# Kernel optimization log

Hardware: AMD Instinct MI355X
Metric: run time of the kernel (lower is better)

The kernel has to match this reference:

```python
import jax, jax.numpy as jnp
import numpy as np

# --- dims / constants ---
T, N, SD, TD, A, H = 64, 512, 64, 64, 32, 2048
REPEAT = 2
IN_DIM = SD + TD
DT, TAU_MEM, TAU_SYN = 1e-3, 5e-3, 2e-3
DCY_M = float(np.exp(-DT / TAU_MEM))   # membrane decay exp(-dt/tau_mem)
DCY_S = float(np.exp(-DT / TAU_SYN))   # synaptic decay exp(-dt/tau_syn)
SCL_M = 1.0 - DCY_M
BETA = 100.0  # SigmoidSpike surrogate steepness

@jax.custom_vjp
def spike(x):
    # forward: hard threshold (binary spike)
    return (x > 0).astype(x.dtype)

def _spike_fwd(x):
    return spike(x), x

def _spike_bwd(x, g):
    s = jax.nn.sigmoid(BETA * x)
    return (g * BETA * s * (1.0 - s),)

spike.defvjp(_spike_fwd, _spike_bwd)

def setup_inputs() -> dict:
    key = jax.random.key(0)
    ks = jax.random.split(key, 8)
    f32 = jnp.float32
    state = jax.random.normal(ks[0], (T, N, SD), dtype=f32)
    target = jax.random.normal(ks[1], (T, N, TD), dtype=f32)
    # fluctuation-driven centered-normal init ~ N(0, 1/fan_in)
    Wi = jax.random.normal(ks[2], (IN_DIM, H), dtype=f32) / np.sqrt(IN_DIM)
    bi = jnp.zeros((H,), dtype=f32)
    Vr = jax.random.normal(ks[3], (H, H), dtype=f32) / np.sqrt(H)
    Wf = jax.random.normal(ks[4], (H, H), dtype=f32) / np.sqrt(H)
    bf = jnp.zeros((H,), dtype=f32)
    Wo = jax.random.normal(ks[5], (H, 2 * A), dtype=f32) / np.sqrt(H)
    bo = jnp.zeros((2 * A,), dtype=f32)
    return {"state": state, "target": target, "Wi": Wi, "bi": bi,
            "Vr": Vr, "Wf": Wf, "bf": bf, "Wo": Wo, "bo": bo}

def _run(state, target, Wi, bi, Vr, Wf, bf, Wo, bo):
    x_seq = jnp.concatenate([state, target], axis=-1)        # (T, N, IN_DIM)
    x_seq = jnp.repeat(x_seq, REPEAT, axis=0)                 # (T*REPEAT, N, IN_DIM)

    def step(carry, xt):
        syn1, mem1, s1, syn2, mem2, s2, synr, memr = carry
        # recurrent LIF layer: feedforward + recurrent input
        I1 = xt @ Wi + bi + s1 @ Vr
        nmem1 = (DCY_M * mem1 + SCL_M * syn1) * (1.0 - s1)    # reset by last spikes
        nsyn1 = DCY_S * syn1 + I1
        ns1 = spike(nmem1 - 1.0)                              # threshold = 1
        # feedforward LIF layer
        I2 = ns1 @ Wf + bf
        nmem2 = (DCY_M * mem2 + SCL_M * syn2) * (1.0 - s2)
        nsyn2 = DCY_S * syn2 + I2
        ns2 = spike(nmem2 - 1.0)
        # non-spiking readout pool (leaky integrator)
        Ir = ns2 @ Wo + bo
        nmemr = DCY_M * memr + SCL_M * synr
        nsynr = DCY_S * synr + Ir
        new_carry = (nsyn1, nmem1, ns1, nsyn2, nmem2, ns2, nsynr, nmemr)
        return new_carry, nmemr

    z = lambda d: jnp.zeros((N, d), dtype=state.dtype)
    carry0 = (z(H), z(H), z(H), z(H), z(H), z(H), z(2 * A), z(2 * A))
    _, ro = jax.lax.scan(step, carry0, x_seq)                 # (T*REPEAT, N, 2A)
    # TimeAverageReadoutGroup: mean over the repeat_input micro-steps
    ro = ro.reshape(T, REPEAT, N, 2 * A).mean(axis=1)         # (T, N, 2A)
    mu, logvar = jnp.split(ro, 2, axis=-1)
    return mu, logvar

def reference(state, target, Wi, bi, Vr, Wf, bf, Wo, bo):
    return _run(state, target, Wi, bi, Vr, Wf, bf, Wo, bo)
```

## Files before the change

### kernel.cpp

```cpp
#include <hip/hip_runtime.h>
#include <stdint.h>


typedef unsigned long long u64;
typedef unsigned int u32;
typedef float f32x4 __attribute__((ext_vector_type(4)));

#define NB 512
#define HD 2048
#define NSTEPS 128
#define THREADS 512
#define NBLK 256
#define COLS 256
#define SPB 16
#define NWPS 32
#define LSTN 1024

#define DMc 0.8187307530779818f
#define DSc 0.6065306597126334f
#define SMc 0.18126924692201818f

#define OFF_M1W 0
#define SZ_M1W (2 * NB * NWPS * 8)
#define OFF_M2H (OFF_M1W + SZ_M1W)
#define SZ_M2H ((size_t)NSTEPS * NB * NWPS * 8)
#define OFF_FLAG (OFF_M2H + SZ_M2H)
#define SZ_FLAG (32 * 32 * 4)
#define OFF_CNT (OFF_FLAG + SZ_FLAG)
#define OFF_DONE (OFF_CNT + 64)
#define OFF_PK (((size_t)(OFF_DONE + 4) + 4194303) & ~(size_t)4194303)
#define SZ_PK ((size_t)8 * HD * 512 * 4)

#define HWREG_XCC_ID (20 | ((4 - 1) << 11))

__global__ void init_ws(u64* __restrict__ m1W, u32* __restrict__ flags,
                        u32* __restrict__ cnt, u32* __restrict__ done) {
  int i = blockIdx.x * 256 + threadIdx.x;
  if (i < 2 * NB * NWPS) m1W[i] = 0ULL;
  if (i < 32 * 32) flags[i] = 0u;
  if (i < 8) cnt[i] = 0u;
  if (i == 0) *done = 0u;
}

__global__ __launch_bounds__(256) void pack_kernel(
    const float* __restrict__ Vr, const float* __restrict__ Wf,
    float* __restrict__ PK) {
  const int k = blockIdx.x;
  const int tid = threadIdx.x;
  for (int c = tid; c < HD; c += 256) {
    int xcd = c >> 8, cc = c & 255;
    size_t base = ((size_t)xcd * HD + k) * 512;
    __builtin_nontemporal_store(Vr[(size_t)k * HD + c], &PK[base + cc]);
    __builtin_nontemporal_store(Wf[(size_t)k * HD + c], &PK[base + 256 + cc]);
  }
}

__device__ __forceinline__ u64 spread4(u64 x) {
  x &= 0xffffULL;
  x = (x | (x << 24)) & 0x000000FF000000FFULL;
  x = (x | (x << 12)) & 0x000F000F000F000FULL;
  x = (x | (x << 6))  & 0x0303030303030303ULL;
  x = (x | (x << 3))  & 0x1111111111111111ULL;
  return x;
}

__device__ __forceinline__ u64 pack_word(u64 B0, u64 B1, u64 B2, u64 B3, int q) {
  int sh = q * 16;
  return spread4(B0 >> sh) | (spread4(B1 >> sh) << 1) |
         (spread4(B2 >> sh) << 2) | (spread4(B3 >> sh) << 3);
}

template <bool ATOMIC>
__device__ __forceinline__ int build_list(const u64* __restrict__ mwords,
                                          uint16_t* __restrict__ lstw, int lane) {
  u64 w = 0ULL;
  if (lane < NWPS) {
    if (ATOMIC)
      w = __hip_atomic_load((u64*)&mwords[lane], __ATOMIC_RELAXED,
                            __HIP_MEMORY_SCOPE_AGENT);
    else
      w = mwords[lane];
  }
  int pc = __popcll(w);
  int pre = pc;
#pragma unroll
  for (int off = 1; off < 64; off <<= 1) {
    int v = __shfl_up(pre, off);
    if (lane >= off) pre += v;
  }
  int excl = pre - pc;
  int total = __shfl(pre, 63);
  int kb = lane << 6;
  while (w) {
    int b = __builtin_ctzll(w);
    w &= w - 1;
    if (excl < LSTN) lstw[excl] = (uint16_t)(kb + b);
    ++excl;
  }
  asm volatile("s_waitcnt lgkmcnt(0)" ::: "memory");
  return total < LSTN ? total : LSTN;
}

__device__ __forceinline__ void dual_gather_pk(const float* __restrict__ PKb,
                                               const uint16_t* __restrict__ lstw,
                                               int total, float aV[4],
                                               float aW[4]) {
  for (int j0 = 0; j0 < total; j0 += 8) {
    f32x4 va[8], vb[8];
#pragma unroll
    for (int u = 0; u < 8; ++u) {
      int idx = j0 + u;
      if (idx >= total) idx = j0;
      size_t off = ((size_t)lstw[idx]) << 9;
      va[u] = *(const f32x4*)(PKb + off);
      vb[u] = *(const f32x4*)(PKb + off + 256);
    }
#pragma unroll
    for (int u = 0; u < 8; ++u)
      if (j0 + u < total) {
        aV[0] += va[u].x; aV[1] += va[u].y; aV[2] += va[u].z; aV[3] += va[u].w;
        aW[0] += vb[u].x; aW[1] += vb[u].y; aW[2] += vb[u].z; aW[3] += vb[u].w;
      }
  }
}

__device__ __forceinline__ u32 lif_update(const float acc[4], float syn[4],
                                          float mem[4], u32 snib) {
  u32 nib = 0;
#pragma unroll
  for (int j = 0; j < 4; ++j) {
    float so = (float)((snib >> j) & 1u);
    float nmem = (DMc * mem[j] + SMc * syn[j]) * (1.0f - so);
    float nsyn = DSc * syn[j] + acc[j];
    mem[j] = nmem;
    syn[j] = nsyn;
    if ((nmem - 1.0f) > 0.0f) nib |= (1u << j);
  }
  return nib;
}

__global__ __launch_bounds__(THREADS) void rsnn_coop(
    const float* __restrict__ state, const float* __restrict__ target,
    const float* __restrict__ Wi, const float* __restrict__ bi,
    const float* __restrict__ Vr, const float* __restrict__ Wf,
    const float* __restrict__ bf, const float* __restrict__ Wo,
    const float* __restrict__ bo, float* __restrict__ out,
    char* __restrict__ wsb) {
  __shared__ float Wi_s[128 * COLS];
  __shared__ uint16_t lst[8][LSTN];
  __shared__ int sh_xcd, sh_rank;

  u64* m1W = (u64*)(wsb + OFF_M1W);
  u64* m2H = (u64*)(wsb + OFF_M2H);
  u32* flags = (u32*)(wsb + OFF_FLAG);
  u32* cnt = (u32*)(wsb + OFF_CNT);
  u32* done = (u32*)(wsb + OFF_DONE);
  const float* PK = (const float*)(wsb + OFF_PK);

  const int tid = threadIdx.x;
  const int wv = tid >> 6;
  const int lane = tid & 63;

  if (tid == 0) {
    int xcd = __builtin_amdgcn_s_getreg(HWREG_XCC_ID) & 7;
    sh_xcd = xcd;
    sh_rank = atomicAdd(&cnt[xcd], 1u) & 31;
  }
  __syncthreads();
  const int xcd = sh_xcd;
  const int g = sh_rank;
  const int c0 = xcd * COLS;
  const int sA = g * SPB + wv * 2, sB = sA + 1;

  for (int i = tid; i < 128 * COLS; i += THREADS) {
    int k = i >> 8, c = i & 255;
    Wi_s[i] = Wi[(size_t)k * HD + c0 + c];
  }

  float bir[4], bfr[4];
#pragma unroll
  for (int j = 0; j < 4; ++j) {
    bir[j] = bi[c0 + lane * 4 + j];
    bfr[j] = bf[c0 + lane * 4 + j];
  }

  float syn1[2][4], mem1[2][4], syn2[2][4], mem2[2][4];
#pragma unroll
  for (int r = 0; r < 2; ++r)
#pragma unroll
    for (int j = 0; j < 4; ++j) {
      syn1[r][j] = 0.f; mem1[r][j] = 0.f; syn2[r][j] = 0.f; mem2[r][j] = 0.f;
    }
  u32 s1nib[2] = {0u, 0u}, s2nib[2] = {0u, 0u};
  float xwA[4], xwB[4];

  const float* PKb = PK + (size_t)xcd * HD * 512 + lane * 4;
  u32* myflag = &flags[g * 32];

  __syncthreads();

  auto compute_xw = [&](int t2) {
#pragma unroll
    for (int j = 0; j < 4; ++j) { xwA[j] = bir[j]; xwB[j] = bir[j]; }
#pragma unroll
    for (int half = 0; half < 2; ++half) {
      const float* pA = (half ? target : state) + ((size_t)t2 * NB + sA) * 64;
      const float* pB = (half ? target : state) + ((size_t)t2 * NB + sB) * 64;
      for (int q = 0; q < 16; ++q) {
        f32x4 xa = *(const f32x4*)(pA + 4 * q);
        f32x4 xb = *(const f32x4*)(pB + 4 * q);
        float xav[4] = {xa.x, xa.y, xa.z, xa.w};
        float xbv[4] = {xb.x, xb.y, xb.z, xb.w};
#pragma unroll
        for (int kj = 0; kj < 4; ++kj) {
          const f32x4 w4 =
              *(const f32x4*)&Wi_s[(half * 64 + 4 * q + kj) * COLS + lane * 4];
          xwA[0] = fmaf(xav[kj], w4.x, xwA[0]);
          xwA[1] = fmaf(xav[kj], w4.y, xwA[1]);
          xwA[2] = fmaf(xav[kj], w4.z, xwA[2]);
          xwA[3] = fmaf(xav[kj], w4.w, xwA[3]);
          xwB[0] = fmaf(xbv[kj], w4.x, xwB[0]);
          xwB[1] = fmaf(xbv[kj], w4.y, xwB[1]);
          xwB[2] = fmaf(xbv[kj], w4.z, xwB[2]);
          xwB[3] = fmaf(xbv[kj], w4.w, xwB[3]);
        }
      }
    }
  };

  compute_xw(0);
#pragma unroll
  for (int r = 0; r < 2; ++r) {
    const int smp = r ? sB : sA;
    s1nib[r] = lif_update(r ? xwB : xwA, syn1[r], mem1[r], s1nib[r]);
    u64 B0 = __ballot(s1nib[r] & 1u), B1 = __ballot(s1nib[r] & 2u);
    u64 B2 = __ballot(s1nib[r] & 4u), B3 = __ballot(s1nib[r] & 8u);
    if (lane < 4) {
      u64 wd = pack_word(B0, B1, B2, B3, lane);
      __hip_atomic_store(&m1W[(size_t)smp * NWPS + 4 * xcd + lane], wd,
                         __ATOMIC_RELAXED, __HIP_MEMORY_SCOPE_AGENT);
    }
  }
  __syncthreads();
  if (tid == 0) {
    __hip_atomic_fetch_add(myflag, 1u, __ATOMIC_RELAXED, __HIP_MEMORY_SCOPE_AGENT);
    while (__hip_atomic_load(myflag, __ATOMIC_RELAXED,
                             __HIP_MEMORY_SCOPE_AGENT) < 8u)
      __builtin_amdgcn_s_sleep(2);
  }
  __syncthreads();

  for (int s = 0; s < NSTEPS; ++s) {
    if (s + 1 < NSTEPS && ((s + 1) & 1) == 0) compute_xw((s + 1) >> 1);

    const u64* m1cur = m1W + (size_t)(s & 1) * NB * NWPS;
    u64* m1nxt = m1W + (size_t)((s + 1) & 1) * NB * NWPS;
    const bool last = (s == NSTEPS - 1);

#pragma unroll
    for (int r = 0; r < 2; ++r) {
      const int smp = r ? sB : sA;
      int tot = build_list<true>(m1cur + (size_t)smp * NWPS, &lst[wv][0], lane);

      float aV[4], aW[4];
#pragma unroll
      for (int j = 0; j < 4; ++j) {
        aV[j] = r ? xwB[j] : xwA[j];
        aW[j] = bfr[j];
      }
      dual_gather_pk(PKb, &lst[wv][0], tot, aV, aW);

      s2nib[r] = lif_update(aW, syn2[r], mem2[r], s2nib[r]);
      {
        u64 B0 = __ballot(s2nib[r] & 1u), B1 = __ballot(s2nib[r] & 2u);
        u64 B2 = __ballot(s2nib[r] & 4u), B3 = __ballot(s2nib[r] & 8u);
        if (lane < 4) {
          u64 wd = pack_word(B0, B1, B2, B3, lane);
          __hip_atomic_store(
              &m2H[((size_t)s * NB + smp) * NWPS + 4 * xcd + lane], wd,
              __ATOMIC_RELAXED, __HIP_MEMORY_SCOPE_AGENT);
        }
      }
      if (!last) {
        s1nib[r] = lif_update(aV, syn1[r], mem1[r], s1nib[r]);
        u64 B0 = __ballot(s1nib[r] & 1u), B1 = __ballot(s1nib[r] & 2u);
        u64 B2 = __ballot(s1nib[r] & 4u), B3 = __ballot(s1nib[r] & 8u);
        if (lane < 4) {
          u64 wd = pack_word(B0, B1, B2, B3, lane);
          __hip_atomic_store(&m1nxt[(size_t)smp * NWPS + 4 * xcd + lane], wd,
                             __ATOMIC_RELAXED, __HIP_MEMORY_SCOPE_AGENT);
        }
      }
    }

    if (!last) {
      __syncthreads();
      if (tid == 0) {
        __hip_atomic_fetch_add(myflag, 1u, __ATOMIC_RELAXED,
                               __HIP_MEMORY_SCOPE_AGENT);
        u32 tgt = 8u * (u32)(s + 2);
        while (__hip_atomic_load(myflag, __ATOMIC_RELAXED,
                                 __HIP_MEMORY_SCOPE_AGENT) < tgt)
          __builtin_amdgcn_s_sleep(2);
      }
      __syncthreads();
    }
  }

  __syncthreads();
  if (tid == 0) {
    __threadfence();
    __hip_atomic_fetch_add(done, 1u, __ATOMIC_RELEASE, __HIP_MEMORY_SCOPE_AGENT);
    while (__hip_atomic_load(done, __ATOMIC_RELAXED,
                             __HIP_MEMORY_SCOPE_AGENT) < (u32)NBLK)
      __builtin_amdgcn_s_sleep(8);
    __threadfence();
  }
  __syncthreads();

  if (wv < 2) {
    const int rsmp = blockIdx.x * 2 + wv;
    const float bor = bo[lane];
    float synr = 0.f, memr = 0.f, roprev = 0.f;
    for (int s = 0; s < NSTEPS; ++s) {
      int total = build_list<false>(m2H + ((size_t)s * NB + rsmp) * NWPS,
                                    &lst[wv][0], lane);
      float a = bor;
      for (int j0 = 0; j0 < total; j0 += 8) {
        float vv[8];
#pragma unroll
        for (int u = 0; u < 8; ++u) {
          int idx = j0 + u;
          if (idx >= total) idx = j0;
          vv[u] = Wo[(((size_t)lst[wv][idx]) << 6) + lane];
        }
#pragma unroll
        for (int u = 0; u < 8; ++u)
          if (j0 + u < total) a += vv[u];
      }
      float nmemr = DMc * memr + SMc * synr;
      float nsynr = DSc * synr + a;
      memr = nmemr;
      synr = nsynr;
      if (s & 1) {
        float v = 0.5f * (roprev + nmemr);
        size_t base = ((size_t)(s >> 1) * NB + rsmp) * 32;
        if (lane < 32) out[base + lane] = v;
        else out[(size_t)64 * NB * 32 + base + (lane - 32)] = v;
      } else {
        roprev = nmemr;
      }
    }
  }
}

extern "C" void kernel_launch(void* const* d_in, const int* in_sizes, int n_in,
                              void* d_out, int out_size, void* d_ws, size_t ws_size,
                              hipStream_t stream) {
  const float* state  = (const float*)d_in[0];
  const float* target = (const float*)d_in[1];
  const float* Wi     = (const float*)d_in[2];
  const float* bi     = (const float*)d_in[3];
  const float* Vr     = (const float*)d_in[4];
  const float* Wf     = (const float*)d_in[5];
  const float* bf     = (const float*)d_in[6];
  const float* Wo     = (const float*)d_in[7];
  const float* bo     = (const float*)d_in[8];
  float* out = (float*)d_out;
  char* wsb = (char*)d_ws;

  init_ws<<<128, 256, 0, stream>>>((u64*)(wsb + OFF_M1W), (u32*)(wsb + OFF_FLAG),
                                   (u32*)(wsb + OFF_CNT), (u32*)(wsb + OFF_DONE));
  pack_kernel<<<HD, 256, 0, stream>>>(Vr, Wf, (float*)(wsb + OFF_PK));

  void* args[] = {(void*)&state, (void*)&target, (void*)&Wi, (void*)&bi,
                  (void*)&Vr, (void*)&Wf, (void*)&bf, (void*)&Wo, (void*)&bo,
                  (void*)&out, (void*)&wsb};
  (void)hipLaunchCooperativeKernel(rsnn_coop, dim3(NBLK), dim3(THREADS), args, 0,
                                   stream);
}
```

Before: 3.688 ms.

## Replace block barriers with per-sample sequence flags and software-pipeline the gather

Drops the per-step block-wide syncthreads plus counter-flag barrier. Each wave now writes its spike words followed by a per-(sample, XCD) sequence-number flag, and waits only on the eight flags for its own samples. It also builds both samples' spike lists in one pass, double-buffers the gathered PK loads, moves the input projection after the step, and shrinks the list size to fit two list buffers. The aim is to remove block-level serialization and expose memory parallelism. The cost is more polling traffic, reliance on relaxed ordering with vmcnt waits for correctness, and higher register pressure.

```diff
diff --git a/kernel.cpp b/kernel.cpp
--- a/kernel.cpp
+++ b/kernel.cpp
@@ -14,30 +14,27 @@
 #define COLS 256
 #define SPB 16
 #define NWPS 32
-#define LSTN 1024
+#define LSTN 832
 
 #define DMc 0.8187307530779818f
 #define DSc 0.6065306597126334f
 #define SMc 0.18126924692201818f
 
 #define OFF_M1W 0
-#define SZ_M1W (2 * NB * NWPS * 8)
+#define SZ_M1W ((size_t)2 * NB * 8 * 8 * 8)
 #define OFF_M2H (OFF_M1W + SZ_M1W)
 #define SZ_M2H ((size_t)NSTEPS * NB * NWPS * 8)
-#define OFF_FLAG (OFF_M2H + SZ_M2H)
-#define SZ_FLAG (32 * 32 * 4)
-#define OFF_CNT (OFF_FLAG + SZ_FLAG)
+#define OFF_CNT (OFF_M2H + SZ_M2H)
 #define OFF_DONE (OFF_CNT + 64)
 #define OFF_PK (((size_t)(OFF_DONE + 4) + 4194303) & ~(size_t)4194303)
 #define SZ_PK ((size_t)8 * HD * 512 * 4)
 
 #define HWREG_XCC_ID (20 | ((4 - 1) << 11))
 
-__global__ void init_ws(u64* __restrict__ m1W, u32* __restrict__ flags,
-                        u32* __restrict__ cnt, u32* __restrict__ done) {
+__global__ void init_ws(u64* __restrict__ m1W, u32* __restrict__ cnt,
+                        u32* __restrict__ done) {
   int i = blockIdx.x * 256 + threadIdx.x;
-  if (i < 2 * NB * NWPS) m1W[i] = 0ULL;
-  if (i < 32 * 32) flags[i] = 0u;
+  if (i < 2 * NB * 64) m1W[i] = 0ULL;
   if (i < 8) cnt[i] = 0u;
   if (i == 0) *done = 0u;
 }
@@ -70,17 +67,10 @@
          (spread4(B2 >> sh) << 2) | (spread4(B3 >> sh) << 3);
 }
 
-template <bool ATOMIC>
-__device__ __forceinline__ int build_list(const u64* __restrict__ mwords,
-                                          uint16_t* __restrict__ lstw, int lane) {
-  u64 w = 0ULL;
-  if (lane < NWPS) {
-    if (ATOMIC)
-      w = __hip_atomic_load((u64*)&mwords[lane], __ATOMIC_RELAXED,
-                            __HIP_MEMORY_SCOPE_AGENT);
-    else
-      w = mwords[lane];
-  }
+__device__ __forceinline__ int build_list_ro(const u64* __restrict__ mwords,
+                                             uint16_t* __restrict__ lstw,
+                                             int lane) {
+  u64 w = (lane < NWPS) ? mwords[lane] : 0ULL;
   int pc = __popcll(w);
   int pre = pc;
 #pragma unroll
@@ -101,29 +91,6 @@
   return total < LSTN ? total : LSTN;
 }
 
-__device__ __forceinline__ void dual_gather_pk(const float* __restrict__ PKb,
-                                               const uint16_t* __restrict__ lstw,
-                                               int total, float aV[4],
-                                               float aW[4]) {
-  for (int j0 = 0; j0 < total; j0 += 8) {
-    f32x4 va[8], vb[8];
-#pragma unroll
-    for (int u = 0; u < 8; ++u) {
-      int idx = j0 + u;
-      if (idx >= total) idx = j0;
-      size_t off = ((size_t)lstw[idx]) << 9;
-      va[u] = *(const f32x4*)(PKb + off);
-      vb[u] = *(const f32x4*)(PKb + off + 256);
-    }
-#pragma unroll
-    for (int u = 0; u < 8; ++u)
-      if (j0 + u < total) {
-        aV[0] += va[u].x; aV[1] += va[u].y; aV[2] += va[u].z; aV[3] += va[u].w;
-        aW[0] += vb[u].x; aW[1] += vb[u].y; aW[2] += vb[u].z; aW[3] += vb[u].w;
-      }
-  }
-}
-
 __device__ __forceinline__ u32 lif_update(const float acc[4], float syn[4],
                                           float mem[4], u32 snib) {
   u32 nib = 0;
@@ -139,7 +106,57 @@
   return nib;
 }
 
-__global__ __launch_bounds__(THREADS) void rsnn_coop(
+__device__ __forceinline__ void dual_gather_pipe(const float* __restrict__ PKb,
+                                                 const uint16_t* __restrict__ lstw,
+                                                 int tot, float aV[4],
+                                                 float aW[4]) {
+  if (tot <= 0) return;
+  f32x4 vaX[8], vbX[8], vaY[8], vbY[8];
+#define LOADG(VA, VB, J)                                      \
+  {                                                           \
+    _Pragma("unroll") for (int u = 0; u < 8; ++u) {           \
+      int idx = (J) + u;                                      \
+      if (idx >= tot) idx = 0;                                \
+      size_t off = ((size_t)lstw[idx]) << 9;                  \
+      VA[u] = *(const f32x4*)(PKb + off);                     \
+      VB[u] = *(const f32x4*)(PKb + off + 256);               \
+    }                                                         \
+  }
+#define ACCG(VA, VB, J)                                       \
+  {                                                           \
+    _Pragma("unroll") for (int u = 0; u < 8; ++u)             \
+      if ((J) + u < tot) {                                    \
+        aV[0] += VA[u].x; aV[1] += VA[u].y;                   \
+        aV[2] += VA[u].z; aV[3] += VA[u].w;                   \
+        aW[0] += VB[u].x; aW[1] += VB[u].y;                   \
+        aW[2] += VB[u].z; aW[3] += VB[u].w;                   \
+      }                                                       \
+  }
+  int j = 0;
+  LOADG(vaX, vbX, 0);
+  while (true) {
+    if (j + 8 < tot) {
+      LOADG(vaY, vbY, j + 8);
+      ACCG(vaX, vbX, j);
+      j += 8;
+    } else {
+      ACCG(vaX, vbX, j);
+      break;
+    }
+    if (j + 8 < tot) {
+      LOADG(vaX, vbX, j + 8);
+      ACCG(vaY, vbY, j);
+      j += 8;
+    } else {
+      ACCG(vaY, vbY, j);
+      break;
+    }
+  }
+#undef LOADG
+#undef ACCG
+}
+
+__global__ __launch_bounds__(THREADS, 2) void rsnn_coop(
     const float* __restrict__ state, const float* __restrict__ target,
     const float* __restrict__ Wi, const float* __restrict__ bi,
     const float* __restrict__ Vr, const float* __restrict__ Wf,
@@ -147,12 +164,12 @@
     const float* __restrict__ bo, float* __restrict__ out,
     char* __restrict__ wsb) {
   __shared__ float Wi_s[128 * COLS];
-  __shared__ uint16_t lst[8][LSTN];
+  __shared__ uint16_t lstA_s[8][LSTN];
+  __shared__ uint16_t lstB_s[8][LSTN];
   __shared__ int sh_xcd, sh_rank;
 
   u64* m1W = (u64*)(wsb + OFF_M1W);
   u64* m2H = (u64*)(wsb + OFF_M2H);
-  u32* flags = (u32*)(wsb + OFF_FLAG);
   u32* cnt = (u32*)(wsb + OFF_CNT);
   u32* done = (u32*)(wsb + OFF_DONE);
   const float* PK = (const float*)(wsb + OFF_PK);
@@ -162,9 +179,9 @@
   const int lane = tid & 63;
 
   if (tid == 0) {
-    int xcd = __builtin_amdgcn_s_getreg(HWREG_XCC_ID) & 7;
-    sh_xcd = xcd;
-    sh_rank = atomicAdd(&cnt[xcd], 1u) & 31;
+    int x = __builtin_amdgcn_s_getreg(HWREG_XCC_ID) & 7;
+    sh_xcd = x;
+    sh_rank = atomicAdd(&cnt[x], 1u) & 31;
   }
   __syncthreads();
   const int xcd = sh_xcd;
@@ -184,18 +201,19 @@
     bfr[j] = bf[c0 + lane * 4 + j];
   }
 
-  float syn1[2][4], mem1[2][4], syn2[2][4], mem2[2][4];
-#pragma unroll
-  for (int r = 0; r < 2; ++r)
-#pragma unroll
-    for (int j = 0; j < 4; ++j) {
-      syn1[r][j] = 0.f; mem1[r][j] = 0.f; syn2[r][j] = 0.f; mem2[r][j] = 0.f;
-    }
-  u32 s1nib[2] = {0u, 0u}, s2nib[2] = {0u, 0u};
+  float syn1A[4], mem1A[4], syn2A[4], mem2A[4];
+  float syn1B[4], mem1B[4], syn2B[4], mem2B[4];
+#pragma unroll
+  for (int j = 0; j < 4; ++j) {
+    syn1A[j] = 0.f; mem1A[j] = 0.f; syn2A[j] = 0.f; mem2A[j] = 0.f;
+    syn1B[j] = 0.f; mem1B[j] = 0.f; syn2B[j] = 0.f; mem2B[j] = 0.f;
+  }
+  u32 nib1A = 0u, nib1B = 0u, nib2A = 0u, nib2B = 0u;
   float xwA[4], xwB[4];
 
   const float* PKb = PK + (size_t)xcd * HD * 512 + lane * 4;
-  u32* myflag = &flags[g * 32];
+  uint16_t* lstA = &lstA_s[wv][0];
+  uint16_t* lstB = &lstB_s[wv][0];
 
   __syncthreads();
 
@@ -229,82 +247,125 @@
   };
 
   compute_xw(0);
-#pragma unroll
-  for (int r = 0; r < 2; ++r) {
-    const int smp = r ? sB : sA;
-    s1nib[r] = lif_update(r ? xwB : xwA, syn1[r], mem1[r], s1nib[r]);
-    u64 B0 = __ballot(s1nib[r] & 1u), B1 = __ballot(s1nib[r] & 2u);
-    u64 B2 = __ballot(s1nib[r] & 4u), B3 = __ballot(s1nib[r] & 8u);
+  nib1A = lif_update(xwA, syn1A, mem1A, 0u);
+  nib1B = lif_update(xwB, syn1B, mem1B, 0u);
+  {
+    u64 E0 = __ballot(nib1A & 1u), E1 = __ballot(nib1A & 2u);
+    u64 E2 = __ballot(nib1A & 4u), E3 = __ballot(nib1A & 8u);
+    u64 F0 = __ballot(nib1B & 1u), F1 = __ballot(nib1B & 2u);
+    u64 F2 = __ballot(nib1B & 4u), F3 = __ballot(nib1B & 8u);
     if (lane < 4) {
-      u64 wd = pack_word(B0, B1, B2, B3, lane);
-      __hip_atomic_store(&m1W[(size_t)smp * NWPS + 4 * xcd + lane], wd,
+      __hip_atomic_store(&m1W[((size_t)sA * 8 + xcd) * 8 + lane],
+                         pack_word(E0, E1, E2, E3, lane), __ATOMIC_RELAXED,
+                         __HIP_MEMORY_SCOPE_AGENT);
+    } else if (lane < 8) {
+      __hip_atomic_store(&m1W[((size_t)sB * 8 + xcd) * 8 + (lane - 4)],
+                         pack_word(F0, F1, F2, F3, lane - 4), __ATOMIC_RELAXED,
+                         __HIP_MEMORY_SCOPE_AGENT);
+    }
+    asm volatile("s_waitcnt vmcnt(0)" ::: "memory");
+    if (lane < 2) {
+      const int smp = lane ? sB : sA;
+      __hip_atomic_store(&m1W[((size_t)smp * 8 + xcd) * 8 + 4], (u64)1,
                          __ATOMIC_RELAXED, __HIP_MEMORY_SCOPE_AGENT);
     }
   }
-  __syncthreads();
-  if (tid == 0) {
-    __hip_atomic_fetch_add(myflag, 1u, __ATOMIC_RELAXED, __HIP_MEMORY_SCOPE_AGENT);
-    while (__hip_atomic_load(myflag, __ATOMIC_RELAXED,
-                             __HIP_MEMORY_SCOPE_AGENT) < 8u)
-      __builtin_amdgcn_s_sleep(2);
-  }
-  __syncthreads();
 
   for (int s = 0; s < NSTEPS; ++s) {
-    if (s + 1 < NSTEPS && ((s + 1) & 1) == 0) compute_xw((s + 1) >> 1);
-
-    const u64* m1cur = m1W + (size_t)(s & 1) * NB * NWPS;
-    u64* m1nxt = m1W + (size_t)((s + 1) & 1) * NB * NWPS;
+    u64* m1p = m1W + (size_t)(s & 1) * NB * 64;
+    u64* m1n = m1W + (size_t)((s + 1) & 1) * NB * 64;
     const bool last = (s == NSTEPS - 1);
 
-#pragma unroll
-    for (int r = 0; r < 2; ++r) {
-      const int smp = r ? sB : sA;
-      int tot = build_list<true>(m1cur + (size_t)smp * NWPS, &lst[wv][0], lane);
-
-      float aV[4], aW[4];
-#pragma unroll
-      for (int j = 0; j < 4; ++j) {
-        aV[j] = r ? xwB[j] : xwA[j];
-        aW[j] = bfr[j];
-      }
-      dual_gather_pk(PKb, &lst[wv][0], tot, aV, aW);
-
-      s2nib[r] = lif_update(aW, syn2[r], mem2[r], s2nib[r]);
-      {
-        u64 B0 = __ballot(s2nib[r] & 1u), B1 = __ballot(s2nib[r] & 2u);
-        u64 B2 = __ballot(s2nib[r] & 4u), B3 = __ballot(s2nib[r] & 8u);
-        if (lane < 4) {
-          u64 wd = pack_word(B0, B1, B2, B3, lane);
-          __hip_atomic_store(
-              &m2H[((size_t)s * NB + smp) * NWPS + 4 * xcd + lane], wd,
-              __ATOMIC_RELAXED, __HIP_MEMORY_SCOPE_AGENT);
-        }
-      }
-      if (!last) {
-        s1nib[r] = lif_update(aV, syn1[r], mem1[r], s1nib[r]);
-        u64 B0 = __ballot(s1nib[r] & 1u), B1 = __ballot(s1nib[r] & 2u);
-        u64 B2 = __ballot(s1nib[r] & 4u), B3 = __ballot(s1nib[r] & 8u);
-        if (lane < 4) {
-          u64 wd = pack_word(B0, B1, B2, B3, lane);
-          __hip_atomic_store(&m1nxt[(size_t)smp * NWPS + 4 * xcd + lane], wd,
-                             __ATOMIC_RELAXED, __HIP_MEMORY_SCOPE_AGENT);
-        }
+    if (lane < 16) {
+      const int smp = (lane < 8) ? sA : sB;
+      u64* sp = m1p + ((size_t)smp * 8 + (lane & 7)) * 8 + 4;
+      while (__hip_atomic_load(sp, __ATOMIC_RELAXED,
+                               __HIP_MEMORY_SCOPE_AGENT) != (u64)(s + 1))
+        __builtin_amdgcn_s_sleep(1);
+    }
+
+    int totA, totB;
+    {
+      const int hf = lane >> 5, wl = lane & 31;
+      const int smp2 = hf ? sB : sA;
+      u64 w = __hip_atomic_load(
+          m1p + ((size_t)smp2 * 8 + (wl >> 2)) * 8 + (wl & 3),
+          __ATOMIC_RELAXED, __HIP_MEMORY_SCOPE_AGENT);
+      int pc = __popcll(w);
+      int pre = pc;
+#pragma unroll
+      for (int off = 1; off < 32; off <<= 1) {
+        int v = __shfl_up(pre, off, 32);
+        if (wl >= off) pre += v;
+      }
+      int excl = pre - pc;
+      totA = __shfl(pre, 31);
+      totB = __shfl(pre, 63);
+      uint16_t* lw = hf ? lstB : lstA;
+      int kb = wl << 6;
+      while (w) {
+        int b = __builtin_ctzll(w);
+        w &= w - 1;
+        if (excl < LSTN) lw[excl] = (uint16_t)(kb + b);
+        ++excl;
+      }
+      asm volatile("s_waitcnt lgkmcnt(0)" ::: "memory");
+      totA = totA < LSTN ? totA : LSTN;
+      totB = totB < LSTN ? totB : LSTN;
+    }
+
+    {
+      float aV[4] = {xwA[0], xwA[1], xwA[2], xwA[3]};
+      float aW[4] = {bfr[0], bfr[1], bfr[2], bfr[3]};
+      dual_gather_pipe(PKb, lstA, totA, aV, aW);
+      nib2A = lif_update(aW, syn2A, mem2A, nib2A);
+      if (!last) nib1A = lif_update(aV, syn1A, mem1A, nib1A);
+      u64 D0 = __ballot(nib2A & 1u), D1 = __ballot(nib2A & 2u);
+      u64 D2 = __ballot(nib2A & 4u), D3 = __ballot(nib2A & 8u);
+      u64 E0 = __ballot(nib1A & 1u), E1 = __ballot(nib1A & 2u);
+      u64 E2 = __ballot(nib1A & 4u), E3 = __ballot(nib1A & 8u);
+      if (lane < 4) {
+        __hip_atomic_store(&m2H[((size_t)s * NB + sA) * NWPS + 4 * xcd + lane],
+                           pack_word(D0, D1, D2, D3, lane), __ATOMIC_RELAXED,
+                           __HIP_MEMORY_SCOPE_AGENT);
+        if (!last)
+          __hip_atomic_store(&m1n[((size_t)sA * 8 + xcd) * 8 + lane],
+                             pack_word(E0, E1, E2, E3, lane), __ATOMIC_RELAXED,
+                             __HIP_MEMORY_SCOPE_AGENT);
+      }
+    }
+
+    {
+      float aV[4] = {xwB[0], xwB[1], xwB[2], xwB[3]};
+      float aW[4] = {bfr[0], bfr[1], bfr[2], bfr[3]};
+      dual_gather_pipe(PKb, lstB, totB, aV, aW);
+      nib2B = lif_update(aW, syn2B, mem2B, nib2B);
+      if (!last) nib1B = lif_update(aV, syn1B, mem1B, nib1B);
+      u64 D0 = __ballot(nib2B & 1u), D1 = __ballot(nib2B & 2u);
+      u64 D2 = __ballot(nib2B & 4u), D3 = __ballot(nib2B & 8u);
+      u64 E0 = __ballot(nib1B & 1u), E1 = __ballot(nib1B & 2u);
+      u64 E2 = __ballot(nib1B & 4u), E3 = __ballot(nib1B & 8u);
+      if (lane < 4) {
+        __hip_atomic_store(&m2H[((size_t)s * NB + sB) * NWPS + 4 * xcd + lane],
+                           pack_word(D0, D1, D2, D3, lane), __ATOMIC_RELAXED,
+                           __HIP_MEMORY_SCOPE_AGENT);
+        if (!last)
+          __hip_atomic_store(&m1n[((size_t)sB * 8 + xcd) * 8 + lane],
+                             pack_word(E0, E1, E2, E3, lane), __ATOMIC_RELAXED,
+                             __HIP_MEMORY_SCOPE_AGENT);
       }
     }
 
     if (!last) {
-      __syncthreads();
-      if (tid == 0) {
-        __hip_atomic_fetch_add(myflag, 1u, __ATOMIC_RELAXED,
-                               __HIP_MEMORY_SCOPE_AGENT);
-        u32 tgt = 8u * (u32)(s + 2);
-        while (__hip_atomic_load(myflag, __ATOMIC_RELAXED,
-                                 __HIP_MEMORY_SCOPE_AGENT) < tgt)
-          __builtin_amdgcn_s_sleep(2);
-      }
-      __syncthreads();
-    }
+      asm volatile("s_waitcnt vmcnt(0)" ::: "memory");
+      if (lane < 2) {
+        const int smp = lane ? sB : sA;
+        __hip_atomic_store(&m1n[((size_t)smp * 8 + xcd) * 8 + 4], (u64)(s + 2),
+                           __ATOMIC_RELAXED, __HIP_MEMORY_SCOPE_AGENT);
+      }
+    }
+
+    if (((s & 1) == 0) && (s + 2 < NSTEPS)) compute_xw((s + 2) >> 1);
   }
 
   __syncthreads();
@@ -323,8 +384,7 @@
     const float bor = bo[lane];
     float synr = 0.f, memr = 0.f, roprev = 0.f;
     for (int s = 0; s < NSTEPS; ++s) {
-      int total = build_list<false>(m2H + ((size_t)s * NB + rsmp) * NWPS,
-                                    &lst[wv][0], lane);
+      int total = build_list_ro(m2H + ((size_t)s * NB + rsmp) * NWPS, lstA, lane);
       float a = bor;
       for (int j0 = 0; j0 < total; j0 += 8) {
         float vv[8];
@@ -332,7 +392,7 @@
         for (int u = 0; u < 8; ++u) {
           int idx = j0 + u;
           if (idx >= total) idx = j0;
-          vv[u] = Wo[(((size_t)lst[wv][idx]) << 6) + lane];
+          vv[u] = Wo[(((size_t)lstA[idx]) << 6) + lane];
         }
 #pragma unroll
         for (int u = 0; u < 8; ++u)
@@ -369,8 +429,8 @@
   float* out = (float*)d_out;
   char* wsb = (char*)d_ws;
 
-  init_ws<<<128, 256, 0, stream>>>((u64*)(wsb + OFF_M1W), (u32*)(wsb + OFF_FLAG),
-                                   (u32*)(wsb + OFF_CNT), (u32*)(wsb + OFF_DONE));
+  init_ws<<<256, 256, 0, stream>>>((u64*)(wsb + OFF_M1W), (u32*)(wsb + OFF_CNT),
+                                   (u32*)(wsb + OFF_DONE));
   pack_kernel<<<HD, 256, 0, stream>>>(Vr, Wf, (float*)(wsb + OFF_PK));
 
   void* args[] = {(void*)&state, (void*)&target, (void*)&Wi, (void*)&bi,
```

After: 5.167 ms. 40.1% more time.

## Precompute input projection in separate kernel and interleave two-sample spike gathers

Applied to the files above, without the earlier changes.

Adds a standalone kernel that precomputes x@Wi+bi for all timesteps into workspace, so the recurrent kernel prefetches it one step ahead instead of doing the projection inside the serial loop. The per-wave list build and gather now handle both samples together, issuing loads for A and B in one loop to raise memory-level parallelism. The list length is reduced and launch bounds allow two blocks per CU. This costs a large extra workspace buffer (with a fallback path if it is too small) and an extra kernel launch.

```diff
diff --git a/kernel.cpp b/kernel.cpp
--- a/kernel.cpp
+++ b/kernel.cpp
@@ -14,14 +14,14 @@
 #define COLS 256
 #define SPB 16
 #define NWPS 32
-#define LSTN 1024
+#define LSTN 832
 
 #define DMc 0.8187307530779818f
 #define DSc 0.6065306597126334f
 #define SMc 0.18126924692201818f
 
 #define OFF_M1W 0
-#define SZ_M1W (2 * NB * NWPS * 8)
+#define SZ_M1W ((size_t)2 * NB * NWPS * 8)
 #define OFF_M2H (OFF_M1W + SZ_M1W)
 #define SZ_M2H ((size_t)NSTEPS * NB * NWPS * 8)
 #define OFF_FLAG (OFF_M2H + SZ_M2H)
@@ -30,6 +30,8 @@
 #define OFF_DONE (OFF_CNT + 64)
 #define OFF_PK (((size_t)(OFF_DONE + 4) + 4194303) & ~(size_t)4194303)
 #define SZ_PK ((size_t)8 * HD * 512 * 4)
+#define OFF_XW (((OFF_PK + SZ_PK) + 255) & ~(size_t)255)
+#define SZ_XW ((size_t)64 * NB * HD * 4)
 
 #define HWREG_XCC_ID (20 | ((4 - 1) << 11))
 
@@ -55,6 +57,39 @@
   }
 }
 
+__global__ __launch_bounds__(256) void xw_kernel(
+    const float* __restrict__ state, const float* __restrict__ target,
+    const float* __restrict__ Wi, const float* __restrict__ bi,
+    float* __restrict__ XW) {
+  __shared__ float xl[16][128];
+  const int tid = threadIdx.x;
+  const int col = blockIdx.x * 256 + tid;
+  const int r0 = blockIdx.y * 16;
+
+  for (int idx = tid; idx < 16 * 128; idx += 256) {
+    int r = idx >> 7, k = idx & 127;
+    int gg = r0 + r;
+    int t = gg >> 9, n = gg & 511;
+    float v = (k < 64) ? state[((size_t)(t * NB + n)) * 64 + k]
+                       : target[((size_t)(t * NB + n)) * 64 + (k - 64)];
+    xl[r][k] = v;
+  }
+  __syncthreads();
+
+  float acc[16];
+  float b = bi[col];
+#pragma unroll
+  for (int r = 0; r < 16; ++r) acc[r] = b;
+  for (int k = 0; k < 128; ++k) {
+    float w = Wi[(size_t)k * HD + col];
+#pragma unroll
+    for (int r = 0; r < 16; ++r) acc[r] = fmaf(xl[r][k], w, acc[r]);
+  }
+#pragma unroll
+  for (int r = 0; r < 16; ++r)
+    __builtin_nontemporal_store(acc[r], &XW[(size_t)(r0 + r) * HD + col]);
+}
+
 __device__ __forceinline__ u64 spread4(u64 x) {
   x &= 0xffffULL;
   x = (x | (x << 24)) & 0x000000FF000000FFULL;
@@ -70,17 +105,42 @@
          (spread4(B2 >> sh) << 2) | (spread4(B3 >> sh) << 3);
 }
 
-template <bool ATOMIC>
-__device__ __forceinline__ int build_list(const u64* __restrict__ mwords,
-                                          uint16_t* __restrict__ lstw, int lane) {
-  u64 w = 0ULL;
-  if (lane < NWPS) {
-    if (ATOMIC)
-      w = __hip_atomic_load((u64*)&mwords[lane], __ATOMIC_RELAXED,
+__device__ __forceinline__ void build_ab(const u64* __restrict__ mA,
+                                         const u64* __restrict__ mB,
+                                         uint16_t* __restrict__ lstA,
+                                         uint16_t* __restrict__ lstB,
+                                         int lane, int& totA, int& totB) {
+  const int hf = lane >> 5, wl = lane & 31;
+  const u64* src = hf ? mB : mA;
+  u64 w = __hip_atomic_load(src + wl, __ATOMIC_RELAXED,
                             __HIP_MEMORY_SCOPE_AGENT);
-    else
-      w = mwords[lane];
-  }
+  int pc = __popcll(w);
+  int pre = pc;
+#pragma unroll
+  for (int off = 1; off < 32; off <<= 1) {
+    int v = __shfl_up(pre, off, 32);
+    if (wl >= off) pre += v;
+  }
+  int excl = pre - pc;
+  totA = __shfl(pre, 31);
+  totB = __shfl(pre, 63);
+  uint16_t* lw = hf ? lstB : lstA;
+  int kb = wl << 6;
+  while (w) {
+    int b = __builtin_ctzll(w);
+    w &= w - 1;
+    if (excl < LSTN) lw[excl] = (uint16_t)(kb + b);
+    ++excl;
+  }
+  asm volatile("s_waitcnt lgkmcnt(0)" ::: "memory");
+  totA = totA < LSTN ? totA : LSTN;
+  totB = totB < LSTN ? totB : LSTN;
+}
+
+__device__ __forceinline__ int build_list_ro(const u64* __restrict__ mwords,
+                                             uint16_t* __restrict__ lstw,
+                                             int lane) {
+  u64 w = (lane < NWPS) ? mwords[lane] : 0ULL;
   int pc = __popcll(w);
   int pre = pc;
 #pragma unroll
@@ -101,29 +161,6 @@
   return total < LSTN ? total : LSTN;
 }
 
-__device__ __forceinline__ void dual_gather_pk(const float* __restrict__ PKb,
-                                               const uint16_t* __restrict__ lstw,
-                                               int total, float aV[4],
-                                               float aW[4]) {
-  for (int j0 = 0; j0 < total; j0 += 8) {
-    f32x4 va[8], vb[8];
-#pragma unroll
-    for (int u = 0; u < 8; ++u) {
-      int idx = j0 + u;
-      if (idx >= total) idx = j0;
-      size_t off = ((size_t)lstw[idx]) << 9;
-      va[u] = *(const f32x4*)(PKb + off);
-      vb[u] = *(const f32x4*)(PKb + off + 256);
-    }
-#pragma unroll
-    for (int u = 0; u < 8; ++u)
-      if (j0 + u < total) {
-        aV[0] += va[u].x; aV[1] += va[u].y; aV[2] += va[u].z; aV[3] += va[u].w;
-        aW[0] += vb[u].x; aW[1] += vb[u].y; aW[2] += vb[u].z; aW[3] += vb[u].w;
-      }
-  }
-}
-
 __device__ __forceinline__ u32 lif_update(const float acc[4], float syn[4],
                                           float mem[4], u32 snib) {
   u32 nib = 0;
@@ -139,7 +176,48 @@
   return nib;
 }
 
-__global__ __launch_bounds__(THREADS) void rsnn_coop(
+__device__ __forceinline__ void gather_ab(const float* __restrict__ PKb,
+                                          const uint16_t* __restrict__ lstA,
+                                          int totA,
+                                          const uint16_t* __restrict__ lstB,
+                                          int totB, float aVA[4], float aWA[4],
+                                          float aVB[4], float aWB[4]) {
+  int tot = totA > totB ? totA : totB;
+  for (int j0 = 0; j0 < tot; j0 += 8) {
+    f32x4 va[8], wa[8], vb[8], wb[8];
+#pragma unroll
+    for (int u = 0; u < 8; ++u) {
+      int ia = j0 + u;
+      if (ia >= totA) ia = 0;
+      size_t offA = ((size_t)lstA[ia]) << 9;
+      va[u] = *(const f32x4*)(PKb + offA);
+      wa[u] = *(const f32x4*)(PKb + offA + 256);
+    }
+#pragma unroll
+    for (int u = 0; u < 8; ++u) {
+      int ib = j0 + u;
+      if (ib >= totB) ib = 0;
+      size_t offB = ((size_t)lstB[ib]) << 9;
+      vb[u] = *(const f32x4*)(PKb + offB);
+      wb[u] = *(const f32x4*)(PKb + offB + 256);
+    }
+#pragma unroll
+    for (int u = 0; u < 8; ++u)
+      if (j0 + u < totA) {
+        aVA[0] += va[u].x; aVA[1] += va[u].y; aVA[2] += va[u].z; aVA[3] += va[u].w;
+        aWA[0] += wa[u].x; aWA[1] += wa[u].y; aWA[2] += wa[u].z; aWA[3] += wa[u].w;
+      }
+#pragma unroll
+    for (int u = 0; u < 8; ++u)
+      if (j0 + u < totB) {
+        aVB[0] += vb[u].x; aVB[1] += vb[u].y; aVB[2] += vb[u].z; aVB[3] += vb[u].w;
+        aWB[0] += wb[u].x; aWB[1] += wb[u].y; aWB[2] += wb[u].z; aWB[3] += wb[u].w;
+      }
+  }
+}
+
+template <int UXW>
+__global__ __launch_bounds__(THREADS, 2) void rsnn_coop(
     const float* __restrict__ state, const float* __restrict__ target,
     const float* __restrict__ Wi, const float* __restrict__ bi,
     const float* __restrict__ Vr, const float* __restrict__ Wf,
@@ -147,7 +225,8 @@
     const float* __restrict__ bo, float* __restrict__ out,
     char* __restrict__ wsb) {
   __shared__ float Wi_s[128 * COLS];
-  __shared__ uint16_t lst[8][LSTN];
+  __shared__ uint16_t lstA_s[8][LSTN];
+  __shared__ uint16_t lstB_s[8][LSTN];
   __shared__ int sh_xcd, sh_rank;
 
   u64* m1W = (u64*)(wsb + OFF_M1W);
@@ -156,15 +235,16 @@
   u32* cnt = (u32*)(wsb + OFF_CNT);
   u32* done = (u32*)(wsb + OFF_DONE);
   const float* PK = (const float*)(wsb + OFF_PK);
+  const float* XW = (const float*)(wsb + OFF_XW);
 
   const int tid = threadIdx.x;
   const int wv = tid >> 6;
   const int lane = tid & 63;
 
   if (tid == 0) {
-    int xcd = __builtin_amdgcn_s_getreg(HWREG_XCC_ID) & 7;
-    sh_xcd = xcd;
-    sh_rank = atomicAdd(&cnt[xcd], 1u) & 31;
+    int x = __builtin_amdgcn_s_getreg(HWREG_XCC_ID) & 7;
+    sh_xcd = x;
+    sh_rank = atomicAdd(&cnt[x], 1u) & 31;
   }
   __syncthreads();
   const int xcd = sh_xcd;
@@ -172,10 +252,15 @@
   const int c0 = xcd * COLS;
   const int sA = g * SPB + wv * 2, sB = sA + 1;
 
-  for (int i = tid; i < 128 * COLS; i += THREADS) {
-    int k = i >> 8, c = i & 255;
-    Wi_s[i] = Wi[(size_t)k * HD + c0 + c];
-  }
+  if constexpr (!UXW) {
+    for (int i = tid; i < 128 * COLS; i += THREADS) {
+      int k = i >> 8, c = i & 255;
+      Wi_s[i] = Wi[(size_t)k * HD + c0 + c];
+    }
+  }
+  uint16_t* lstA = &lstA_s[wv][0];
+  uint16_t* lstB = &lstB_s[wv][0];
+  if (lane == 0) { lstA[0] = 0; lstB[0] = 0; }
 
   float bir[4], bfr[4];
 #pragma unroll
@@ -184,17 +269,19 @@
     bfr[j] = bf[c0 + lane * 4 + j];
   }
 
-  float syn1[2][4], mem1[2][4], syn2[2][4], mem2[2][4];
-#pragma unroll
-  for (int r = 0; r < 2; ++r)
-#pragma unroll
-    for (int j = 0; j < 4; ++j) {
-      syn1[r][j] = 0.f; mem1[r][j] = 0.f; syn2[r][j] = 0.f; mem2[r][j] = 0.f;
-    }
-  u32 s1nib[2] = {0u, 0u}, s2nib[2] = {0u, 0u};
+  float syn1A[4], mem1A[4], syn2A[4], mem2A[4];
+  float syn1B[4], mem1B[4], syn2B[4], mem2B[4];
+#pragma unroll
+  for (int j = 0; j < 4; ++j) {
+    syn1A[j] = 0.f; mem1A[j] = 0.f; syn2A[j] = 0.f; mem2A[j] = 0.f;
+    syn1B[j] = 0.f; mem1B[j] = 0.f; syn2B[j] = 0.f; mem2B[j] = 0.f;
+  }
+  u32 nib1A = 0u, nib1B = 0u, nib2A = 0u, nib2B = 0u;
   float xwA[4], xwB[4];
+  f32x4 xwNA, xwNB;
 
   const float* PKb = PK + (size_t)xcd * HD * 512 + lane * 4;
+  const float* XWc = XW + c0 + lane * 4;
   u32* myflag = &flags[g * 32];
 
   __syncthreads();
@@ -228,18 +315,35 @@
     }
   };
 
-  compute_xw(0);
-#pragma unroll
-  for (int r = 0; r < 2; ++r) {
-    const int smp = r ? sB : sA;
-    s1nib[r] = lif_update(r ? xwB : xwA, syn1[r], mem1[r], s1nib[r]);
-    u64 B0 = __ballot(s1nib[r] & 1u), B1 = __ballot(s1nib[r] & 2u);
-    u64 B2 = __ballot(s1nib[r] & 4u), B3 = __ballot(s1nib[r] & 8u);
-    if (lane < 4) {
-      u64 wd = pack_word(B0, B1, B2, B3, lane);
-      __hip_atomic_store(&m1W[(size_t)smp * NWPS + 4 * xcd + lane], wd,
-                         __ATOMIC_RELAXED, __HIP_MEMORY_SCOPE_AGENT);
-    }
+  if constexpr (UXW) {
+    f32x4 a = __builtin_nontemporal_load((const f32x4*)(XWc + (size_t)sA * HD));
+    f32x4 b = __builtin_nontemporal_load((const f32x4*)(XWc + (size_t)sB * HD));
+    xwA[0] = a.x; xwA[1] = a.y; xwA[2] = a.z; xwA[3] = a.w;
+    xwB[0] = b.x; xwB[1] = b.y; xwB[2] = b.z; xwB[3] = b.w;
+  } else {
+    compute_xw(0);
+  }
+  nib1A = lif_update(xwA, syn1A, mem1A, 0u);
+  nib1B = lif_update(xwB, syn1B, mem1B, 0u);
+  {
+    u64 E0 = __ballot(nib1A & 1u), E1 = __ballot(nib1A & 2u);
+    u64 E2 = __ballot(nib1A & 4u), E3 = __ballot(nib1A & 8u);
+    u64 F0 = __ballot(nib1B & 1u), F1 = __ballot(nib1B & 2u);
+    u64 F2 = __ballot(nib1B & 4u), F3 = __ballot(nib1B & 8u);
+    if (lane < 4)
+      __hip_atomic_store(&m1W[(size_t)sA * NWPS + 4 * xcd + lane],
+                         pack_word(E0, E1, E2, E3, lane), __ATOMIC_RELAXED,
+                         __HIP_MEMORY_SCOPE_AGENT);
+    else if (lane < 8)
+      __hip_atomic_store(&m1W[(size_t)sB * NWPS + 4 * xcd + (lane - 4)],
+                         pack_word(F0, F1, F2, F3, lane - 4), __ATOMIC_RELAXED,
+                         __HIP_MEMORY_SCOPE_AGENT);
+  }
+  if constexpr (UXW) {
+    xwNA = __builtin_nontemporal_load(
+        (const f32x4*)(XWc + ((size_t)1 * NB + sA) * HD));
+    xwNB = __builtin_nontemporal_load(
+        (const f32x4*)(XWc + ((size_t)1 * NB + sB) * HD));
   }
   __syncthreads();
   if (tid == 0) {
@@ -251,45 +355,72 @@
   __syncthreads();
 
   for (int s = 0; s < NSTEPS; ++s) {
-    if (s + 1 < NSTEPS && ((s + 1) & 1) == 0) compute_xw((s + 1) >> 1);
+    if (s & 1) {
+      if constexpr (UXW) {
+        xwA[0] = xwNA.x; xwA[1] = xwNA.y; xwA[2] = xwNA.z; xwA[3] = xwNA.w;
+        xwB[0] = xwNB.x; xwB[1] = xwNB.y; xwB[2] = xwNB.z; xwB[3] = xwNB.w;
+      } else {
+        if (s + 1 < NSTEPS) compute_xw((s + 1) >> 1);
+      }
+    } else {
+      if constexpr (UXW) {
+        int t2 = (s >> 1) + 1;
+        if (t2 < 64) {
+          xwNA = __builtin_nontemporal_load(
+              (const f32x4*)(XWc + ((size_t)t2 * NB + sA) * HD));
+          xwNB = __builtin_nontemporal_load(
+              (const f32x4*)(XWc + ((size_t)t2 * NB + sB) * HD));
+        }
+      }
+    }
 
     const u64* m1cur = m1W + (size_t)(s & 1) * NB * NWPS;
-    u64* m1nxt = m1W + (size_t)((s + 1) & 1) * NB * NWPS;
+    u64* m1n = m1W + (size_t)((s + 1) & 1) * NB * NWPS;
     const bool last = (s == NSTEPS - 1);
 
-#pragma unroll
-    for (int r = 0; r < 2; ++r) {
-      const int smp = r ? sB : sA;
-      int tot = build_list<true>(m1cur + (size_t)smp * NWPS, &lst[wv][0], lane);
-
-      float aV[4], aW[4];
-#pragma unroll
-      for (int j = 0; j < 4; ++j) {
-        aV[j] = r ? xwB[j] : xwA[j];
-        aW[j] = bfr[j];
-      }
-      dual_gather_pk(PKb, &lst[wv][0], tot, aV, aW);
-
-      s2nib[r] = lif_update(aW, syn2[r], mem2[r], s2nib[r]);
-      {
-        u64 B0 = __ballot(s2nib[r] & 1u), B1 = __ballot(s2nib[r] & 2u);
-        u64 B2 = __ballot(s2nib[r] & 4u), B3 = __ballot(s2nib[r] & 8u);
-        if (lane < 4) {
-          u64 wd = pack_word(B0, B1, B2, B3, lane);
-          __hip_atomic_store(
-              &m2H[((size_t)s * NB + smp) * NWPS + 4 * xcd + lane], wd,
-              __ATOMIC_RELAXED, __HIP_MEMORY_SCOPE_AGENT);
-        }
-      }
+    int totA, totB;
+    build_ab(m1cur + (size_t)sA * NWPS, m1cur + (size_t)sB * NWPS, lstA, lstB,
+             lane, totA, totB);
+
+    float aVA[4] = {xwA[0], xwA[1], xwA[2], xwA[3]};
+    float aWA[4] = {bfr[0], bfr[1], bfr[2], bfr[3]};
+    float aVB[4] = {xwB[0], xwB[1], xwB[2], xwB[3]};
+    float aWB[4] = {bfr[0], bfr[1], bfr[2], bfr[3]};
+    gather_ab(PKb, lstA, totA, lstB, totB, aVA, aWA, aVB, aWB);
+
+    nib2A = lif_update(aWA, syn2A, mem2A, nib2A);
+    nib2B = lif_update(aWB, syn2B, mem2B, nib2B);
+    if (!last) {
+      nib1A = lif_update(aVA, syn1A, mem1A, nib1A);
+      nib1B = lif_update(aVB, syn1B, mem1B, nib1B);
+    }
+    {
+      u64 D0 = __ballot(nib2A & 1u), D1 = __ballot(nib2A & 2u);
+      u64 D2 = __ballot(nib2A & 4u), D3 = __ballot(nib2A & 8u);
+      u64 G0 = __ballot(nib2B & 1u), G1 = __ballot(nib2B & 2u);
+      u64 G2 = __ballot(nib2B & 4u), G3 = __ballot(nib2B & 8u);
+      if (lane < 4)
+        __hip_atomic_store(&m2H[((size_t)s * NB + sA) * NWPS + 4 * xcd + lane],
+                           pack_word(D0, D1, D2, D3, lane), __ATOMIC_RELAXED,
+                           __HIP_MEMORY_SCOPE_AGENT);
+      else if (lane < 8)
+        __hip_atomic_store(
+            &m2H[((size_t)s * NB + sB) * NWPS + 4 * xcd + (lane - 4)],
+            pack_word(G0, G1, G2, G3, lane - 4), __ATOMIC_RELAXED,
+            __HIP_MEMORY_SCOPE_AGENT);
       if (!last) {
-        s1nib[r] = lif_update(aV, syn1[r], mem1[r], s1nib[r]);
-        u64 B0 = __ballot(s1nib[r] & 1u), B1 = __ballot(s1nib[r] & 2u);
-        u64 B2 = __ballot(s1nib[r] & 4u), B3 = __ballot(s1nib[r] & 8u);
-        if (lane < 4) {
-          u64 wd = pack_word(B0, B1, B2, B3, lane);
-          __hip_atomic_store(&m1nxt[(size_t)smp * NWPS + 4 * xcd + lane], wd,
+        u64 E0 = __ballot(nib1A & 1u), E1 = __ballot(nib1A & 2u);
+        u64 E2 = __ballot(nib1A & 4u), E3 = __ballot(nib1A & 8u);
+        u64 F0 = __ballot(nib1B & 1u), F1 = __ballot(nib1B & 2u);
+        u64 F2 = __ballot(nib1B & 4u), F3 = __ballot(nib1B & 8u);
+        if (lane < 4)
+          __hip_atomic_store(&m1n[(size_t)sA * NWPS + 4 * xcd + lane],
+                             pack_word(E0, E1, E2, E3, lane), __ATOMIC_RELAXED,
+                             __HIP_MEMORY_SCOPE_AGENT);
+        else if (lane < 8)
+          __hip_atomic_store(&m1n[(size_t)sB * NWPS + 4 * xcd + (lane - 4)],
+                             pack_word(F0, F1, F2, F3, lane - 4),
                              __ATOMIC_RELAXED, __HIP_MEMORY_SCOPE_AGENT);
-        }
       }
     }
 
@@ -323,8 +454,7 @@
     const float bor = bo[lane];
     float synr = 0.f, memr = 0.f, roprev = 0.f;
     for (int s = 0; s < NSTEPS; ++s) {
-      int total = build_list<false>(m2H + ((size_t)s * NB + rsmp) * NWPS,
-                                    &lst[wv][0], lane);
+      int total = build_list_ro(m2H + ((size_t)s * NB + rsmp) * NWPS, lstA, lane);
       float a = bor;
       for (int j0 = 0; j0 < total; j0 += 8) {
         float vv[8];
@@ -332,7 +462,7 @@
         for (int u = 0; u < 8; ++u) {
           int idx = j0 + u;
           if (idx >= total) idx = j0;
-          vv[u] = Wo[(((size_t)lst[wv][idx]) << 6) + lane];
+          vv[u] = Wo[(((size_t)lstA[idx]) << 6) + lane];
         }
 #pragma unroll
         for (int u = 0; u < 8; ++u)
@@ -369,13 +499,22 @@
   float* out = (float*)d_out;
   char* wsb = (char*)d_ws;
 
+  const int use_xw = (ws_size >= OFF_XW + SZ_XW) ? 1 : 0;
+
   init_ws<<<128, 256, 0, stream>>>((u64*)(wsb + OFF_M1W), (u32*)(wsb + OFF_FLAG),
                                    (u32*)(wsb + OFF_CNT), (u32*)(wsb + OFF_DONE));
   pack_kernel<<<HD, 256, 0, stream>>>(Vr, Wf, (float*)(wsb + OFF_PK));
+  if (use_xw)
+    xw_kernel<<<dim3(8, 2048), 256, 0, stream>>>(state, target, Wi, bi,
+                                                 (float*)(wsb + OFF_XW));
 
   void* args[] = {(void*)&state, (void*)&target, (void*)&Wi, (void*)&bi,
                   (void*)&Vr, (void*)&Wf, (void*)&bf, (void*)&Wo, (void*)&bo,
                   (void*)&out, (void*)&wsb};
-  (void)hipLaunchCooperativeKernel(rsnn_coop, dim3(NBLK), dim3(THREADS), args, 0,
-                                   stream);
-}
+  if (use_xw)
+    (void)hipLaunchCooperativeKernel(rsnn_coop<1>, dim3(NBLK), dim3(THREADS),
+                                     args, 0, stream);
+  else
+    (void)hipLaunchCooperativeKernel(rsnn_coop<0>, dim3(NBLK), dim3(THREADS),
+                                     args, 0, stream);
+}
```

After: 3.578 ms. 1.03x faster.
